# Kernel optimization log

Hardware: AMD Instinct MI355X
Metric: run time of the kernel (lower is better)

## Reference

```python
import jax, jax.numpy as jnp
import numpy as np
from jax import lax

B, N, S, K = 8, 4096, 1024, 32   # batch, points, npoint (FPS samples), nsample (ball query)
RADIUS = 0.15
ALPHA = 0.2                      # LeakyReLU negative slope
EPS = 1e-5                       # BatchNorm eps
MLP = [64, 64, 128]
D_IN = 6                         # per-point feature dim


def _index_points(p, idx):
    # p: [B, N, C]; idx: [B, ...] -> [B, ..., C]
    return jax.vmap(lambda pp, ii: pp[ii])(p, idx)


def _fps(xyz, npoint):
    # Farthest point sampling. Deterministic start at index 0 (original uses randint).
    b, n, _ = xyz.shape
    def step(carry, _):
        dist, far = carry
        c = xyz[jnp.arange(b), far]                    # [b,3] current centroid
        d = jnp.sum((xyz - c[:, None, :]) ** 2, -1)    # [b,n]
        dist = jnp.minimum(dist, d)
        return (dist, jnp.argmax(dist, -1).astype(jnp.int32)), far
    init = (jnp.full((b, n), 1e10, xyz.dtype), jnp.zeros((b,), jnp.int32))
    _, cent = lax.scan(step, init, None, length=npoint)
    return cent.T                                       # [b, npoint]


def _ball_query(radius, nsample, xyz, new_xyz):
    n = xyz.shape[1]
    # squared distances [B,S,N]
    sqr = (jnp.sum(new_xyz ** 2, -1)[:, :, None]
           + jnp.sum(xyz ** 2, -1)[:, None, :]
           - 2.0 * jnp.einsum('bsc,bnc->bsn', new_xyz, xyz))
    idx = jnp.where(sqr > radius * radius, n,
                    jnp.arange(n, dtype=jnp.int32)[None, None, :])
    idx = jnp.sort(idx, axis=-1)[:, :, :nsample]        # [B,S,K]
    return jnp.where(idx == n, idx[:, :, :1], idx)      # pad misses with first hit


def _mlp_bn_relu(x, w, b, g, be, m, v):
    # 1x1 Conv2d == linear on last axis; BatchNorm in eval mode with running stats.
    x = jnp.einsum('...c,oc->...o', x, w) + b
    x = g * (x - m) * lax.rsqrt(v + EPS) + be
    return jax.nn.relu(x)


def reference(xyz, points, w0, b0, g0, be0, m0, v0, w1, b1, g1, be1, m1, v1,
              w2, b2, g2, be2, m2, v2, a):
    params = [(w0, b0, g0, be0, m0, v0), (w1, b1, g1, be1, m1, v1),
              (w2, b2, g2, be2, m2, v2)]
    xyz_t = xyz.transpose(0, 2, 1)                      # [B,N,3]
    pts = points.transpose(0, 2, 1)                     # [B,N,D]

    fps_idx = _fps(xyz_t, S)                            # [B,S]
    new_xyz = _index_points(xyz_t, fps_idx)             # [B,S,3]
    idx = _ball_query(RADIUS, K, xyz_t, new_xyz)        # [B,S,K]
    grouped_xyz = _index_points(xyz_t, idx)             # [B,S,K,3]
    grouped_pts = _index_points(pts, idx)               # [B,S,K,D]
    fps_pts = _index_points(pts, fps_idx)               # [B,S,D]

    center = jnp.concatenate([new_xyz, fps_pts], -1)                       # [B,S,3+D]
    neigh = jnp.concatenate([grouped_xyz - new_xyz[:, :, None, :],
                             grouped_pts], -1)                             # [B,S,K,3+D]

    for (w, b, g, be, m, v) in params:
        center = _mlp_bn_relu(center, w, b, g, be, m, v)
        neigh = _mlp_bn_relu(neigh, w, b, g, be, m, v)

    # Graph attention: LeakyReLU scores, softmax over neighbors, weighted sum.
    dp = new_xyz[:, :, None, :] - grouped_xyz                              # [B,S,K,3]
    dh = center[:, :, None, :] - neigh                                     # [B,S,K,Dout]
    e = jax.nn.leaky_relu(jnp.concatenate([dp, dh], -1) @ a, ALPHA)        # [B,S,K,Dout]
    att = jax.nn.softmax(e, axis=2)                                        # over K
    out = jnp.sum(att * neigh, axis=2)                                     # [B,S,Dout]

    return new_xyz.transpose(0, 2, 1), out.transpose(0, 2, 1)              # [B,3,S],[B,Dout,S]


def setup_inputs() -> dict:
    key = jax.random.key(0)
    ks = jax.random.split(key, 32)
    inp = {
        'xyz': jax.random.uniform(ks[0], (B, 3, N), jnp.float32),
        'points': jax.random.normal(ks[1], (B, D_IN, N), jnp.float32),
    }
    last = 3 + D_IN
    j = 2
    for i, out_c in enumerate(MLP):
        scale = np.sqrt(2.0 / (last + out_c)).astype(np.float32)
        inp[f'w{i}'] = jax.random.normal(ks[j], (out_c, last), jnp.float32) * scale; j += 1
        inp[f'b{i}'] = jax.random.normal(ks[j], (out_c,), jnp.float32) * 0.01; j += 1
        inp[f'g{i}'] = 1.0 + 0.1 * jax.random.normal(ks[j], (out_c,), jnp.float32); j += 1
        inp[f'be{i}'] = 0.1 * jax.random.normal(ks[j], (out_c,), jnp.float32); j += 1
        inp[f'm{i}'] = 0.1 * jax.random.normal(ks[j], (out_c,), jnp.float32); j += 1
        inp[f'v{i}'] = 0.5 + jax.random.uniform(ks[j], (out_c,), jnp.float32); j += 1
        last = out_c
    inp['a'] = jax.random.normal(ks[j], (3 + MLP[-1], MLP[-1]), jnp.float32) * np.sqrt(2.0 / (3 + 2 * MLP[-1])).astype(np.float32)
    return inp


if __name__ == '__main__':
    o = reference(**setup_inputs())
    print(o[0].shape, o[1].shape)
```

## Files before the change

kernel.cpp:

```cpp
#include <hip/hip_runtime.h>

#define NB  8
#define NPT 4096
#define NS  1024
#define NK  32
#define DIN 6
#define QPB 32
#define MEGA_THREADS 512

#define OFF_A   0
#define OFF_W1  16768
#define OFF_W2  20864
#define OFF_W0  29056
#define OFF_H   29632
#define OFF_U   31808
#define OFF_NB  36032
#define FLT_TOT 36416
#define SMEM_BYTES (FLT_TOT * 4 + (8 * NK + 8 + NK) * 4)

__device__ __forceinline__ float bnrelu(float acc, const float* __restrict__ bb,
                                        const float* __restrict__ gg,
                                        const float* __restrict__ be,
                                        const float* __restrict__ mm,
                                        const float* __restrict__ vv, int oc) {
  float t = (acc + bb[oc]) - mm[oc];
  float val = gg[oc] * t * rsqrtf(vv[oc] + 1e-5f) + be[oc];
  return fmaxf(val, 0.0f);
}

__device__ __forceinline__ float wave64_max(float x) {
  const int NEG1 = 0xbf800000;
  int v;
  v = __builtin_amdgcn_update_dpp(NEG1, __float_as_int(x), 0x111, 0xf, 0xf, false);
  x = fmaxf(x, __int_as_float(v));
  v = __builtin_amdgcn_update_dpp(NEG1, __float_as_int(x), 0x112, 0xf, 0xf, false);
  x = fmaxf(x, __int_as_float(v));
  v = __builtin_amdgcn_update_dpp(NEG1, __float_as_int(x), 0x114, 0xf, 0xf, false);
  x = fmaxf(x, __int_as_float(v));
  v = __builtin_amdgcn_update_dpp(NEG1, __float_as_int(x), 0x118, 0xf, 0xf, false);
  x = fmaxf(x, __int_as_float(v));
  v = __builtin_amdgcn_update_dpp(NEG1, __float_as_int(x), 0x142, 0xa, 0xf, false);
  x = fmaxf(x, __int_as_float(v));
  v = __builtin_amdgcn_update_dpp(NEG1, __float_as_int(x), 0x143, 0xc, 0xf, false);
  x = fmaxf(x, __int_as_float(v));
  return __int_as_float(__builtin_amdgcn_readlane(__float_as_int(x), 63));
}

__global__ __launch_bounds__(512) void fps_kernel(const float* __restrict__ xyz,
                                                  int* __restrict__ fps_idx,
                                                  float* __restrict__ nxyz,
                                                  float* __restrict__ out0) {
  const int b = blockIdx.x;
  const int t = threadIdx.x;
  const int lane = t & 63, wid = t >> 6;
  const float* xb = xyz + (size_t)b * 3 * NPT;

  __shared__ float s_x[NPT], s_y[NPT], s_z[NPT];
  __shared__ __align__(16) float s_red[2][8][2];
  __shared__ float s_ox[NS], s_oy[NS], s_oz[NS];
  __shared__ int s_fi[NS];

  float px[8], py[8], pz[8], dist[8];
  const int base = t * 8;
#pragma unroll
  for (int j = 0; j < 8; ++j) {
    px[j] = xb[base + j];
    py[j] = xb[NPT + base + j];
    pz[j] = xb[2 * NPT + base + j];
    dist[j] = 1e10f;
  }
  for (int i = t; i < NPT; i += 512) {
    s_x[i] = xb[i];
    s_y[i] = xb[NPT + i];
    s_z[i] = xb[2 * NPT + i];
  }
  __syncthreads();

  int far = 0;
  float cx = xb[0], cy = xb[NPT], cz = xb[2 * NPT];

  for (int s = 0; s < NS; ++s) {
    if (t == 0) {
      s_ox[s] = cx; s_oy[s] = cy; s_oz[s] = cz; s_fi[s] = far;
    }
    float bv = -1.0f;
    int bi = 0;
#pragma unroll
    for (int j = 0; j < 8; ++j) {
      float dx = __fsub_rn(px[j], cx);
      float dy = __fsub_rn(py[j], cy);
      float dz = __fsub_rn(pz[j], cz);
      float d = __fadd_rn(__fadd_rn(__fmul_rn(dx, dx), __fmul_rn(dy, dy)),
                          __fmul_rn(dz, dz));
      float nd = fminf(dist[j], d);
      dist[j] = nd;
      bi = (nd > bv) ? (base + j) : bi;
      bv = fmaxf(bv, nd);
    }
    float mv = wave64_max(bv);
    unsigned long long mmask = __ballot(bv == mv);
    int src = __ffsll(mmask) - 1;
    int wi = __shfl(bi, src);

    const int p = s & 1;
    if (lane == 0) {
      s_red[p][wid][0] = mv;
      s_red[p][wid][1] = __int_as_float(wi);
    }
    __syncthreads();

    float4 q0 = *(const float4*)&s_red[p][0][0];
    float4 q1 = *(const float4*)&s_red[p][2][0];
    float4 q2 = *(const float4*)&s_red[p][4][0];
    float4 q3 = *(const float4*)&s_red[p][6][0];
    float rv[8] = {q0.x, q0.z, q1.x, q1.z, q2.x, q2.z, q3.x, q3.z};
    int ri[8] = {__float_as_int(q0.y), __float_as_int(q0.w),
                 __float_as_int(q1.y), __float_as_int(q1.w),
                 __float_as_int(q2.y), __float_as_int(q2.w),
                 __float_as_int(q3.y), __float_as_int(q3.w)};
    float bestv = rv[0];
    int nfar = ri[0];
#pragma unroll
    for (int w = 1; w < 8; ++w) {
      bool better = rv[w] > bestv;
      bestv = better ? rv[w] : bestv;
      nfar = better ? ri[w] : nfar;
    }
    far = nfar;
    cx = s_x[far]; cy = s_y[far]; cz = s_z[far];
  }

  __syncthreads();
  for (int i = t; i < NS; i += 512) {
    float X = s_ox[i], Y = s_oy[i], Z = s_oz[i];
    out0[((size_t)b * 3 + 0) * NS + i] = X;
    out0[((size_t)b * 3 + 1) * NS + i] = Y;
    out0[((size_t)b * 3 + 2) * NS + i] = Z;
    nxyz[((size_t)b * NS + i) * 3 + 0] = X;
    nxyz[((size_t)b * NS + i) * 3 + 1] = Y;
    nxyz[((size_t)b * NS + i) * 3 + 2] = Z;
    fps_idx[b * NS + i] = s_fi[i];
  }
}

__global__ __launch_bounds__(64) void center_kernel(
    const float* __restrict__ points, const float* __restrict__ nxyz,
    const int* __restrict__ fps_idx,
    const float* __restrict__ w0, const float* __restrict__ b0,
    const float* __restrict__ g0, const float* __restrict__ be0,
    const float* __restrict__ m0, const float* __restrict__ v0,
    const float* __restrict__ w1, const float* __restrict__ b1,
    const float* __restrict__ g1, const float* __restrict__ be1,
    const float* __restrict__ m1, const float* __restrict__ v1,
    const float* __restrict__ w2, const float* __restrict__ b2,
    const float* __restrict__ g2, const float* __restrict__ be2,
    const float* __restrict__ m2, const float* __restrict__ v2,
    const float* __restrict__ a, float* __restrict__ ceA) {
  const int bs = blockIdx.x;
  const int b = bs >> 10;
  const int t = threadIdx.x;

  __shared__ float ci[9];
  __shared__ float ch1[64];
  __shared__ float ch2[64];
  __shared__ float ch3[128];

  if (t < 9) {
    ci[t] = (t < 3) ? nxyz[(size_t)bs * 3 + t]
                    : points[((size_t)b * DIN + (t - 3)) * NPT + fps_idx[bs]];
  }
  __syncthreads();
  {
    float acc = 0.f;
#pragma unroll
    for (int c = 0; c < 9; ++c) acc = fmaf(ci[c], w0[t * 9 + c], acc);
    ch1[t] = bnrelu(acc, b0, g0, be0, m0, v0, t);
  }
  __syncthreads();
  {
    float acc = 0.f;
#pragma unroll 8
    for (int c = 0; c < 64; ++c) acc = fmaf(ch1[c], w1[t * 64 + c], acc);
    ch2[t] = bnrelu(acc, b1, g1, be1, m1, v1, t);
  }
  __syncthreads();
  for (int oc = t; oc < 128; oc += 64) {
    float acc = 0.f;
#pragma unroll 8
    for (int c = 0; c < 64; ++c) acc = fmaf(ch2[c], w2[oc * 64 + c], acc);
    ch3[oc] = bnrelu(acc, b2, g2, be2, m2, v2, oc);
  }
  __syncthreads();
  for (int oc = t; oc < 128; oc += 64) {
    float acc = 0.f;
#pragma unroll 8
    for (int c = 0; c < 128; ++c) acc = fmaf(ch3[c], a[(3 + c) * 128 + oc], acc);
    ceA[(size_t)bs * 128 + oc] = acc;
  }
}

__global__ __launch_bounds__(MEGA_THREADS) void mega_kernel(
    const float* __restrict__ xyz, const float* __restrict__ points,
    const float* __restrict__ nxyz, const float* __restrict__ ceA,
    const float* __restrict__ w0, const float* __restrict__ b0,
    const float* __restrict__ g0, const float* __restrict__ be0,
    const float* __restrict__ m0, const float* __restrict__ v0,
    const float* __restrict__ w1, const float* __restrict__ b1,
    const float* __restrict__ g1, const float* __restrict__ be1,
    const float* __restrict__ m1, const float* __restrict__ v1,
    const float* __restrict__ w2, const float* __restrict__ b2,
    const float* __restrict__ g2, const float* __restrict__ be2,
    const float* __restrict__ m2, const float* __restrict__ v2,
    const float* __restrict__ a, float* __restrict__ out1) {
  extern __shared__ float lds[];
  float* s_a  = lds + OFF_A;
  float* s_w1 = lds + OFF_W1;
  float* s_w2 = lds + OFF_W2;
  float* s_w0 = lds + OFF_W0;
  float* s_h  = lds + OFF_H;
  float* s_u  = lds + OFF_U;
  float* s_nb = lds + OFF_NB;
  int* s_widx = (int*)(lds + FLT_TOT);
  int* s_wc   = s_widx + 8 * NK;
  int* s_idx  = s_wc + 8;

  const int t = threadIdx.x;
  const int lane = t & 63;
  const int wvid = t >> 6;
  const int k = t & 31;
  const int g16 = t >> 5;

  {
    const float4* srcA = (const float4*)a;
    float4* dstA = (float4*)s_a;
    for (int i = t; i < 4192; i += MEGA_THREADS) dstA[i] = srcA[i];
    const float4* src1 = (const float4*)w1;
    float4* dst1 = (float4*)s_w1;
    for (int i = t; i < 1024; i += MEGA_THREADS) dst1[i] = src1[i];
    const float4* src2 = (const float4*)w2;
    float4* dst2 = (float4*)s_w2;
    for (int i = t; i < 2048; i += MEGA_THREADS) dst2[i] = src2[i];
    for (int i = t; i < 576; i += MEGA_THREADS) s_w0[i] = w0[i];
  }
  __syncthreads();

  for (int q = 0; q < QPB; ++q) {
    const int bs = blockIdx.x * QPB + q;
    const int b = bs >> 10;
    const int s = bs & 1023;
    const float* xb = xyz + (size_t)b * 3 * NPT;
    const float cx = nxyz[(size_t)bs * 3 + 0];
    const float cy = nxyz[(size_t)bs * 3 + 1];
    const float cz = nxyz[(size_t)bs * 3 + 2];

    {
      const float R2 = (float)(0.15 * 0.15);
      float s2c = __fadd_rn(__fadd_rn(__fmul_rn(cx, cx), __fmul_rn(cy, cy)),
                            __fmul_rn(cz, cz));
      int wcnt = 0;
      for (int g = 0; g < 8; ++g) {
        int n = wvid * 512 + g * 64 + lane;
        float x = xb[n];
        float y = xb[NPT + n];
        float z = xb[2 * NPT + n];
        float pn2 = __fadd_rn(__fadd_rn(__fmul_rn(x, x), __fmul_rn(y, y)),
                              __fmul_rn(z, z));
        float dot = fmaf(cz, z, fmaf(cy, y, __fmul_rn(cx, x)));
        float sqr = __fsub_rn(__fadd_rn(s2c, pn2), __fmul_rn(2.0f, dot));
        bool hit = !(sqr > R2);
        unsigned long long mm = __ballot(hit);
        int pos = wcnt + __popcll(mm & ((1ull << lane) - 1ull));
        if (hit && pos < NK) s_widx[wvid * NK + pos] = n;
        wcnt += __popcll(mm);
        if (wcnt >= NK) break;
      }
      if (lane == 0) s_wc[wvid] = (wcnt < NK) ? wcnt : NK;
    }
    __syncthreads();

    if (t < NK) {
      int cc[8];
#pragma unroll
      for (int w = 0; w < 8; ++w) cc[w] = s_wc[w];
      int total = 0;
#pragma unroll
      for (int w = 0; w < 8; ++w) total += cc[w];
      int p = (t < total) ? t : 0;
      int w = 0;
      while (w < 7 && p >= cc[w]) { p -= cc[w]; ++w; }
      int n = s_widx[w * NK + p];
      s_idx[t] = n;
      s_nb[t * 12 + 0] = __fsub_rn(xb[n], cx);
      s_nb[t * 12 + 1] = __fsub_rn(xb[NPT + n], cy);
      s_nb[t * 12 + 2] = __fsub_rn(xb[2 * NPT + n], cz);
      const float* pb = points + (size_t)b * DIN * NPT + n;
#pragma unroll
      for (int c = 0; c < 6; ++c) s_nb[t * 12 + 3 + c] = pb[(size_t)c * NPT];
      s_nb[t * 12 + 9] = 0.f; s_nb[t * 12 + 10] = 0.f; s_nb[t * 12 + 11] = 0.f;
    }
    __syncthreads();

    {
      const float4* nrow = (const float4*)&s_nb[k * 12];
      float4 r0 = nrow[0], r1 = nrow[1], r2 = nrow[2];
      float in0[9] = {r0.x, r0.y, r0.z, r0.w, r1.x, r1.y, r1.z, r1.w, r2.x};
      int oc0 = g16 * 4;
      float acc[4];
#pragma unroll
      for (int j = 0; j < 4; ++j) {
        float a0 = 0.f;
#pragma unroll
        for (int c = 0; c < 9; ++c)
          a0 = fmaf(in0[c], s_w0[(oc0 + j) * 9 + c], a0);
        acc[j] = bnrelu(a0, b0, g0, be0, m0, v0, oc0 + j);
      }
      *(float4*)&s_h[k * 68 + oc0] = make_float4(acc[0], acc[1], acc[2], acc[3]);
    }
    __syncthreads();

    {
      int oc0 = g16 * 4;
      float acc[4] = {0.f, 0.f, 0.f, 0.f};
      const float4* row = (const float4*)&s_h[k * 68];
#pragma unroll 4
      for (int c4 = 0; c4 < 16; ++c4) {
        float4 hv = row[c4];
#pragma unroll
        for (int j = 0; j < 4; ++j) {
          float4 wv = *(const float4*)&s_w1[(oc0 + j) * 64 + c4 * 4];
          acc[j] = fmaf(hv.x, wv.x, acc[j]);
          acc[j] = fmaf(hv.y, wv.y, acc[j]);
          acc[j] = fmaf(hv.z, wv.z, acc[j]);
          acc[j] = fmaf(hv.w, wv.w, acc[j]);
        }
      }
#pragma unroll
      for (int j = 0; j < 4; ++j)
        acc[j] = bnrelu(acc[j], b1, g1, be1, m1, v1, oc0 + j);
      __syncthreads();
      *(float4*)&s_h[k * 68 + oc0] = make_float4(acc[0], acc[1], acc[2], acc[3]);
    }
    __syncthreads();

    {
      int oc0 = g16 * 8;
      float acc[8] = {0.f, 0.f, 0.f, 0.f, 0.f, 0.f, 0.f, 0.f};
      const float4* row = (const float4*)&s_h[k * 68];
#pragma unroll 2
      for (int c4 = 0; c4 < 16; ++c4) {
        float4 hv = row[c4];
#pragma unroll
        for (int j = 0; j < 8; ++j) {
          float4 wv = *(const float4*)&s_w2[(oc0 + j) * 64 + c4 * 4];
          acc[j] = fmaf(hv.x, wv.x, acc[j]);
          acc[j] = fmaf(hv.y, wv.y, acc[j]);
          acc[j] = fmaf(hv.z, wv.z, acc[j]);
          acc[j] = fmaf(hv.w, wv.w, acc[j]);
        }
      }
#pragma unroll
      for (int j = 0; j < 8; ++j)
        acc[j] = bnrelu(acc[j], b2, g2, be2, m2, v2, oc0 + j);
      float4* orow = (float4*)&s_u[k * 132 + oc0];
      orow[0] = make_float4(acc[0], acc[1], acc[2], acc[3]);
      orow[1] = make_float4(acc[4], acc[5], acc[6], acc[7]);
      if (t < NK) {
        s_u[t * 132 + 128] = s_nb[t * 12 + 0];
        s_u[t * 132 + 129] = s_nb[t * 12 + 1];
        s_u[t * 132 + 130] = s_nb[t * 12 + 2];
        s_u[t * 132 + 131] = 0.f;
      }
    }
    __syncthreads();

    {
      int oc0 = g16 * 8;
      float acc[8] = {0.f, 0.f, 0.f, 0.f, 0.f, 0.f, 0.f, 0.f};
      const float4* urow = (const float4*)&s_u[k * 132];
      for (int r4 = 0; r4 < 33; ++r4) {
        float4 uv = urow[r4];
        int r = r4 * 4;
#pragma unroll
        for (int cc = 0; cc < 4; ++cc) {
          int rr = r + cc;
          int arow = (rr < 128) ? (rr + 3) : (rr - 128);
          float uc = (cc == 0) ? uv.x : (cc == 1) ? uv.y : (cc == 2) ? uv.z : uv.w;
          const float4* ap = (const float4*)&s_a[arow * 128 + oc0];
          float4 av0 = ap[0], av1 = ap[1];
          acc[0] = fmaf(uc, av0.x, acc[0]);
          acc[1] = fmaf(uc, av0.y, acc[1]);
          acc[2] = fmaf(uc, av0.z, acc[2]);
          acc[3] = fmaf(uc, av0.w, acc[3]);
          acc[4] = fmaf(uc, av1.x, acc[4]);
          acc[5] = fmaf(uc, av1.y, acc[5]);
          acc[6] = fmaf(uc, av1.z, acc[6]);
          acc[7] = fmaf(uc, av1.w, acc[7]);
        }
      }

      float ce[8], h3[8];
      {
        float4 cv0 = *(const float4*)&ceA[(size_t)bs * 128 + oc0];
        float4 cv1 = *(const float4*)&ceA[(size_t)bs * 128 + oc0 + 4];
        ce[0] = cv0.x; ce[1] = cv0.y; ce[2] = cv0.z; ce[3] = cv0.w;
        ce[4] = cv1.x; ce[5] = cv1.y; ce[6] = cv1.z; ce[7] = cv1.w;
        float4 hv0 = *(const float4*)&s_u[k * 132 + oc0];
        float4 hv1 = *(const float4*)&s_u[k * 132 + oc0 + 4];
        h3[0] = hv0.x; h3[1] = hv0.y; h3[2] = hv0.z; h3[3] = hv0.w;
        h3[4] = hv1.x; h3[5] = hv1.y; h3[6] = hv1.z; h3[7] = hv1.w;
      }

      float* outb = out1 + (size_t)b * 128 * NS + s;
#pragma unroll
      for (int j = 0; j < 8; ++j) {
        float e = ce[j] - acc[j];
        e = (e >= 0.f) ? e : 0.2f * e;
        float mx = e;
#pragma unroll
        for (int off = 16; off > 0; off >>= 1)
          mx = fmaxf(mx, __shfl_xor(mx, off));
        float p = expf(e - mx);
        float num = p * h3[j];
        float den = p;
#pragma unroll
        for (int off = 16; off > 0; off >>= 1) {
          num += __shfl_xor(num, off);
          den += __shfl_xor(den, off);
        }
        if (k == 0) outb[(size_t)(oc0 + j) * NS] = num / den;
      }
    }
    __syncthreads();
  }
}

extern "C" void kernel_launch(void* const* d_in, const int* in_sizes, int n_in,
                              void* d_out, int out_size, void* d_ws,
                              size_t ws_size, hipStream_t stream) {
  (void)in_sizes; (void)n_in; (void)out_size; (void)ws_size;
  const float* xyz = (const float*)d_in[0];
  const float* points = (const float*)d_in[1];
  const float* w0 = (const float*)d_in[2];
  const float* b0 = (const float*)d_in[3];
  const float* g0 = (const float*)d_in[4];
  const float* be0 = (const float*)d_in[5];
  const float* m0 = (const float*)d_in[6];
  const float* v0 = (const float*)d_in[7];
  const float* w1 = (const float*)d_in[8];
  const float* b1 = (const float*)d_in[9];
  const float* g1 = (const float*)d_in[10];
  const float* be1 = (const float*)d_in[11];
  const float* m1 = (const float*)d_in[12];
  const float* v1 = (const float*)d_in[13];
  const float* w2 = (const float*)d_in[14];
  const float* b2 = (const float*)d_in[15];
  const float* g2 = (const float*)d_in[16];
  const float* be2 = (const float*)d_in[17];
  const float* m2 = (const float*)d_in[18];
  const float* v2 = (const float*)d_in[19];
  const float* a = (const float*)d_in[20];

  float* out0 = (float*)d_out;
  float* out1 = out0 + (size_t)NB * 3 * NS;

  int* fps = (int*)d_ws;
  float* nxyz = (float*)((char*)d_ws + 32768);
  float* ceA = (float*)((char*)d_ws + 32768 + 98304);

  hipFuncSetAttribute(reinterpret_cast<const void*>(mega_kernel),
                      hipFuncAttributeMaxDynamicSharedMemorySize, SMEM_BYTES);

  fps_kernel<<<NB, 512, 0, stream>>>(xyz, fps, nxyz, out0);
  center_kernel<<<NB * NS, 64, 0, stream>>>(points, nxyz, fps,
      w0, b0, g0, be0, m0, v0, w1, b1, g1, be1, m1, v1,
      w2, b2, g2, be2, m2, v2, a, ceA);
  mega_kernel<<<NB * NS / QPB, MEGA_THREADS, SMEM_BYTES, stream>>>(
      xyz, points, nxyz, ceA,
      w0, b0, g0, be0, m0, v0, w1, b1, g1, be1, m1, v1,
      w2, b2, g2, be2, m2, v2, a, out1);
}
```

Before: 1.296 ms.

## Split ball query into separate kernel and trim barriers in MLP megakernel

Moves the ball-query search out of the per-block loop of the megakernel into its own kernel with one 256-thread block per centroid, writing relative coordinates and indices to a workspace buffer. The megakernel then reads neighbours directly into registers. Using separate ping-pong LDS buffers for the hidden layers lets it drop two barriers per query. The FPS argmax reduction also becomes a tree instead of a linear chain. The cost is an extra launch and a global round-trip for the grouped neighbours.

```diff
diff --git a/kernel.cpp b/kernel.cpp
--- a/kernel.cpp
+++ b/kernel.cpp
@@ -12,11 +12,11 @@
 #define OFF_W1  16768
 #define OFF_W2  20864
 #define OFF_W0  29056
-#define OFF_H   29632
-#define OFF_U   31808
-#define OFF_NB  36032
-#define FLT_TOT 36416
-#define SMEM_BYTES (FLT_TOT * 4 + (8 * NK + 8 + NK) * 4)
+#define OFF_H1  29632
+#define OFF_H2  31808
+#define OFF_U   33984
+#define FLT_TOT 38208
+#define SMEM_BYTES (FLT_TOT * 4)
 
 __device__ __forceinline__ float bnrelu(float acc, const float* __restrict__ bb,
                                         const float* __restrict__ gg,
@@ -113,20 +113,19 @@
     float4 q1 = *(const float4*)&s_red[p][2][0];
     float4 q2 = *(const float4*)&s_red[p][4][0];
     float4 q3 = *(const float4*)&s_red[p][6][0];
-    float rv[8] = {q0.x, q0.z, q1.x, q1.z, q2.x, q2.z, q3.x, q3.z};
-    int ri[8] = {__float_as_int(q0.y), __float_as_int(q0.w),
-                 __float_as_int(q1.y), __float_as_int(q1.w),
-                 __float_as_int(q2.y), __float_as_int(q2.w),
-                 __float_as_int(q3.y), __float_as_int(q3.w)};
-    float bestv = rv[0];
-    int nfar = ri[0];
-#pragma unroll
-    for (int w = 1; w < 8; ++w) {
-      bool better = rv[w] > bestv;
-      bestv = better ? rv[w] : bestv;
-      nfar = better ? ri[w] : nfar;
-    }
-    far = nfar;
+    float va, vb, vc, vd; int ia, ib, ic, id;
+    { bool g = q0.z > q0.x; va = g ? q0.z : q0.x;
+      ia = g ? __float_as_int(q0.w) : __float_as_int(q0.y); }
+    { bool g = q1.z > q1.x; vb = g ? q1.z : q1.x;
+      ib = g ? __float_as_int(q1.w) : __float_as_int(q1.y); }
+    { bool g = q2.z > q2.x; vc = g ? q2.z : q2.x;
+      ic = g ? __float_as_int(q2.w) : __float_as_int(q2.y); }
+    { bool g = q3.z > q3.x; vd = g ? q3.z : q3.x;
+      id = g ? __float_as_int(q3.w) : __float_as_int(q3.y); }
+    { bool g = vb > va; va = g ? vb : va; ia = g ? ib : ia; }
+    { bool g = vd > vc; vc = g ? vd : vc; ic = g ? id : ic; }
+    { bool g = vc > va; va = g ? vc : va; ia = g ? ic : ia; }
+    far = ia;
     cx = s_x[far]; cy = s_y[far]; cz = s_z[far];
   }
 
@@ -199,9 +198,66 @@
   }
 }
 
+__global__ __launch_bounds__(256) void ballq_kernel(
+    const float* __restrict__ xyz, const float* __restrict__ nxyz,
+    float4* __restrict__ gq) {
+  const int bs = blockIdx.x;
+  const int b = bs >> 10;
+  const int t = threadIdx.x;
+  const int lane = t & 63;
+  const int wid = t >> 6;
+
+  __shared__ int s_widx[4][NK];
+  __shared__ int s_wc[4];
+
+  const float* xb = xyz + (size_t)b * 3 * NPT;
+  const float cx = nxyz[(size_t)bs * 3 + 0];
+  const float cy = nxyz[(size_t)bs * 3 + 1];
+  const float cz = nxyz[(size_t)bs * 3 + 2];
+
+  {
+    const float R2 = (float)(0.15 * 0.15);
+    float s2c = __fadd_rn(__fadd_rn(__fmul_rn(cx, cx), __fmul_rn(cy, cy)),
+                          __fmul_rn(cz, cz));
+    int wcnt = 0;
+    for (int g = 0; g < 16; ++g) {
+      int n = wid * 1024 + g * 64 + lane;
+      float x = xb[n];
+      float y = xb[NPT + n];
+      float z = xb[2 * NPT + n];
+      float pn2 = __fadd_rn(__fadd_rn(__fmul_rn(x, x), __fmul_rn(y, y)),
+                            __fmul_rn(z, z));
+      float dot = fmaf(cz, z, fmaf(cy, y, __fmul_rn(cx, x)));
+      float sqr = __fsub_rn(__fadd_rn(s2c, pn2), __fmul_rn(2.0f, dot));
+      bool hit = !(sqr > R2);
+      unsigned long long mm = __ballot(hit);
+      int pos = wcnt + __popcll(mm & ((1ull << lane) - 1ull));
+      if (hit && pos < NK) s_widx[wid][pos] = n;
+      wcnt += __popcll(mm);
+      if (wcnt >= NK) break;
+    }
+    if (lane == 0) s_wc[wid] = (wcnt < NK) ? wcnt : NK;
+  }
+  __syncthreads();
+
+  if (t < NK) {
+    int c0 = s_wc[0], c1 = s_wc[1], c2 = s_wc[2], c3 = s_wc[3];
+    int total = c0 + c1 + c2 + c3;
+    int cc[4] = {c0, c1, c2, c3};
+    int p = (t < total) ? t : 0;
+    int w = 0;
+    while (w < 3 && p >= cc[w]) { p -= cc[w]; ++w; }
+    int n = s_widx[w][p];
+    float gx = __fsub_rn(xb[n], cx);
+    float gy = __fsub_rn(xb[NPT + n], cy);
+    float gz = __fsub_rn(xb[2 * NPT + n], cz);
+    gq[(size_t)bs * NK + t] = make_float4(gx, gy, gz, __int_as_float(n));
+  }
+}
+
 __global__ __launch_bounds__(MEGA_THREADS) void mega_kernel(
-    const float* __restrict__ xyz, const float* __restrict__ points,
-    const float* __restrict__ nxyz, const float* __restrict__ ceA,
+    const float* __restrict__ points, const float* __restrict__ ceA,
+    const float4* __restrict__ gq,
     const float* __restrict__ w0, const float* __restrict__ b0,
     const float* __restrict__ g0, const float* __restrict__ be0,
     const float* __restrict__ m0, const float* __restrict__ v0,
@@ -217,16 +273,11 @@
   float* s_w1 = lds + OFF_W1;
   float* s_w2 = lds + OFF_W2;
   float* s_w0 = lds + OFF_W0;
-  float* s_h  = lds + OFF_H;
+  float* s_h1 = lds + OFF_H1;
+  float* s_h2 = lds + OFF_H2;
   float* s_u  = lds + OFF_U;
-  float* s_nb = lds + OFF_NB;
-  int* s_widx = (int*)(lds + FLT_TOT);
-  int* s_wc   = s_widx + 8 * NK;
-  int* s_idx  = s_wc + 8;
 
   const int t = threadIdx.x;
-  const int lane = t & 63;
-  const int wvid = t >> 6;
   const int k = t & 31;
   const int g16 = t >> 5;
 
@@ -248,62 +299,16 @@
     const int bs = blockIdx.x * QPB + q;
     const int b = bs >> 10;
     const int s = bs & 1023;
-    const float* xb = xyz + (size_t)b * 3 * NPT;
-    const float cx = nxyz[(size_t)bs * 3 + 0];
-    const float cy = nxyz[(size_t)bs * 3 + 1];
-    const float cz = nxyz[(size_t)bs * 3 + 2];
+
+    float4 gv = gq[(size_t)bs * NK + k];
+    const int n = __float_as_int(gv.w);
 
     {
-      const float R2 = (float)(0.15 * 0.15);
-      float s2c = __fadd_rn(__fadd_rn(__fmul_rn(cx, cx), __fmul_rn(cy, cy)),
-                            __fmul_rn(cz, cz));
-      int wcnt = 0;
-      for (int g = 0; g < 8; ++g) {
-        int n = wvid * 512 + g * 64 + lane;
-        float x = xb[n];
-        float y = xb[NPT + n];
-        float z = xb[2 * NPT + n];
-        float pn2 = __fadd_rn(__fadd_rn(__fmul_rn(x, x), __fmul_rn(y, y)),
-                              __fmul_rn(z, z));
-        float dot = fmaf(cz, z, fmaf(cy, y, __fmul_rn(cx, x)));
-        float sqr = __fsub_rn(__fadd_rn(s2c, pn2), __fmul_rn(2.0f, dot));
-        bool hit = !(sqr > R2);
-        unsigned long long mm = __ballot(hit);
-        int pos = wcnt + __popcll(mm & ((1ull << lane) - 1ull));
-        if (hit && pos < NK) s_widx[wvid * NK + pos] = n;
-        wcnt += __popcll(mm);
-        if (wcnt >= NK) break;
-      }
-      if (lane == 0) s_wc[wvid] = (wcnt < NK) ? wcnt : NK;
-    }
-    __syncthreads();
-
-    if (t < NK) {
-      int cc[8];
-#pragma unroll
-      for (int w = 0; w < 8; ++w) cc[w] = s_wc[w];
-      int total = 0;
-#pragma unroll
-      for (int w = 0; w < 8; ++w) total += cc[w];
-      int p = (t < total) ? t : 0;
-      int w = 0;
-      while (w < 7 && p >= cc[w]) { p -= cc[w]; ++w; }
-      int n = s_widx[w * NK + p];
-      s_idx[t] = n;
-      s_nb[t * 12 + 0] = __fsub_rn(xb[n], cx);
-      s_nb[t * 12 + 1] = __fsub_rn(xb[NPT + n], cy);
-      s_nb[t * 12 + 2] = __fsub_rn(xb[2 * NPT + n], cz);
+      float in0[9];
+      in0[0] = gv.x; in0[1] = gv.y; in0[2] = gv.z;
       const float* pb = points + (size_t)b * DIN * NPT + n;
 #pragma unroll
-      for (int c = 0; c < 6; ++c) s_nb[t * 12 + 3 + c] = pb[(size_t)c * NPT];
-      s_nb[t * 12 + 9] = 0.f; s_nb[t * 12 + 10] = 0.f; s_nb[t * 12 + 11] = 0.f;
-    }
-    __syncthreads();
-
-    {
-      const float4* nrow = (const float4*)&s_nb[k * 12];
-      float4 r0 = nrow[0], r1 = nrow[1], r2 = nrow[2];
-      float in0[9] = {r0.x, r0.y, r0.z, r0.w, r1.x, r1.y, r1.z, r1.w, r2.x};
+      for (int c = 0; c < 6; ++c) in0[3 + c] = pb[(size_t)c * NPT];
       int oc0 = g16 * 4;
       float acc[4];
 #pragma unroll
@@ -314,14 +319,14 @@
           a0 = fmaf(in0[c], s_w0[(oc0 + j) * 9 + c], a0);
         acc[j] = bnrelu(a0, b0, g0, be0, m0, v0, oc0 + j);
       }
-      *(float4*)&s_h[k * 68 + oc0] = make_float4(acc[0], acc[1], acc[2], acc[3]);
+      *(float4*)&s_h1[k * 68 + oc0] = make_float4(acc[0], acc[1], acc[2], acc[3]);
     }
     __syncthreads();
 
     {
       int oc0 = g16 * 4;
       float acc[4] = {0.f, 0.f, 0.f, 0.f};
-      const float4* row = (const float4*)&s_h[k * 68];
+      const float4* row = (const float4*)&s_h1[k * 68];
 #pragma unroll 4
       for (int c4 = 0; c4 < 16; ++c4) {
         float4 hv = row[c4];
@@ -337,15 +342,14 @@
 #pragma unroll
       for (int j = 0; j < 4; ++j)
         acc[j] = bnrelu(acc[j], b1, g1, be1, m1, v1, oc0 + j);
-      __syncthreads();
-      *(float4*)&s_h[k * 68 + oc0] = make_float4(acc[0], acc[1], acc[2], acc[3]);
+      *(float4*)&s_h2[k * 68 + oc0] = make_float4(acc[0], acc[1], acc[2], acc[3]);
     }
     __syncthreads();
 
     {
       int oc0 = g16 * 8;
       float acc[8] = {0.f, 0.f, 0.f, 0.f, 0.f, 0.f, 0.f, 0.f};
-      const float4* row = (const float4*)&s_h[k * 68];
+      const float4* row = (const float4*)&s_h2[k * 68];
 #pragma unroll 2
       for (int c4 = 0; c4 < 16; ++c4) {
         float4 hv = row[c4];
@@ -365,9 +369,9 @@
       orow[0] = make_float4(acc[0], acc[1], acc[2], acc[3]);
       orow[1] = make_float4(acc[4], acc[5], acc[6], acc[7]);
       if (t < NK) {
-        s_u[t * 132 + 128] = s_nb[t * 12 + 0];
-        s_u[t * 132 + 129] = s_nb[t * 12 + 1];
-        s_u[t * 132 + 130] = s_nb[t * 12 + 2];
+        s_u[t * 132 + 128] = gv.x;
+        s_u[t * 132 + 129] = gv.y;
+        s_u[t * 132 + 130] = gv.z;
         s_u[t * 132 + 131] = 0.f;
       }
     }
@@ -430,7 +434,6 @@
         if (k == 0) outb[(size_t)(oc0 + j) * NS] = num / den;
       }
     }
-    __syncthreads();
   }
 }
 
@@ -465,17 +468,19 @@
 
   int* fps = (int*)d_ws;
   float* nxyz = (float*)((char*)d_ws + 32768);
-  float* ceA = (float*)((char*)d_ws + 32768 + 98304);
+  float* ceA = (float*)((char*)d_ws + 131072);
+  float4* gq = (float4*)((char*)d_ws + 131072 + 4194304);
 
   hipFuncSetAttribute(reinterpret_cast<const void*>(mega_kernel),
                       hipFuncAttributeMaxDynamicSharedMemorySize, SMEM_BYTES);
 
   fps_kernel<<<NB, 512, 0, stream>>>(xyz, fps, nxyz, out0);
+  ballq_kernel<<<NB * NS, 256, 0, stream>>>(xyz, nxyz, gq);
   center_kernel<<<NB * NS, 64, 0, stream>>>(points, nxyz, fps,
       w0, b0, g0, be0, m0, v0, w1, b1, g1, be1, m1, v1,
       w2, b2, g2, be2, m2, v2, a, ceA);
   mega_kernel<<<NB * NS / QPB, MEGA_THREADS, SMEM_BYTES, stream>>>(
-      xyz, points, nxyz, ceA,
+      points, ceA, gq,
       w0, b0, g0, be0, m0, v0, w1, b1, g1, be1, m1, v1,
       w2, b2, g2, be2, m2, v2, a, out1);
 }
```

Result: faster. 1.265 ms (-2.4%).
